# Optimization experiments

Measured on AMD Instinct MI355X. Metric: run time of the kernel, lower is better.

Reference implementation:

```python
import jax, jax.numpy as jnp
import numpy as np

B, N, DEG = 16, 1723, 8   # batch, mesh vertices, avg degree
C, L = 512, 5             # num_channels, num_layers


def _gn(x, g, b, G):
    # GroupNorm over (B, C, N), normalize per group over (C//G, N)
    Bx, Cx, Nx = x.shape
    xr = x.reshape(Bx, G, Cx // G, Nx)
    m = xr.mean(axis=(2, 3), keepdims=True)
    v = xr.var(axis=(2, 3), keepdims=True)
    xr = (xr - m) * jax.lax.rsqrt(v + 1e-5)
    return xr.reshape(Bx, Cx, Nx) * g[None, :, None] + b[None, :, None]


def _glin(W, b, x):
    # per-vertex linear: (O,I) @ (B,I,N) + b
    return jnp.einsum('oi,bin->bon', W, x) + b[None, :, None]


def _gconv(x, W, b, src, dst, w):
    # GraphConvolution: support = x^T @ W, then sparse adjacency spmm via edge list
    sup = jnp.einsum('bcn,cd->bnd', x, W)          # (B, N, C)
    msg = sup[:, src, :] * w[None, :, None]        # gather neighbors (B, E, C)
    agg = jnp.zeros_like(sup).at[:, dst, :].add(msg) + b[None, None, :]
    return agg.transpose(0, 2, 1)                  # back to (B, C, N)


def _resblock(x, p, src, dst, w):
    (pre_g, pre_b, l1W, l1b, n1g, n1b, cW, cb, n2g, n2b, l2W, l2b, skW, skb) = p
    Cin, Ch = x.shape[1], l1W.shape[0]
    y = jax.nn.relu(_gn(x, pre_g, pre_b, Cin // 8))
    y = _glin(l1W, l1b, y)
    y = jax.nn.relu(_gn(y, n1g, n1b, Ch // 8))
    y = _gconv(y, cW, cb, src, dst, w)
    y = jax.nn.relu(_gn(y, n2g, n2b, Ch // 8))
    y = _glin(l2W, l2b, y)
    if skW is not None:
        x = _glin(skW, skb, x)
    return x + y


def setup_inputs() -> dict:
    key = jax.random.key(0)
    ks = iter(jax.random.split(key, 64))
    s = 0.02
    w = lambda shp: jax.random.normal(next(ks), shp, jnp.float32) * s
    z = lambda shp: jnp.zeros(shp, jnp.float32)
    o = lambda shp: jnp.ones(shp, jnp.float32)
    H = C // 2
    E = N * DEG
    inp = {}
    inp['image_resnet'] = jax.random.normal(next(ks), (B, 2048), jnp.float32)
    inp['ref_vertices'] = jax.random.normal(next(ks), (3, N), jnp.float32)
    inp['adj_src'] = jax.random.randint(next(ks), (E,), 0, N, jnp.int32)
    inp['adj_dst'] = jnp.repeat(jnp.arange(N, dtype=jnp.int32), DEG)
    inp['adj_w'] = jnp.full((E,), 1.0 / DEG, jnp.float32)
    inp['lin0_W'] = w((2 * C, 3 + 2048)); inp['lin0_b'] = z((2 * C,))
    inp['b0_pre_g'] = o((2 * C,)); inp['b0_pre_b'] = z((2 * C,))
    inp['b0_lin1_W'] = w((H, 2 * C)); inp['b0_lin1_b'] = z((H,))
    inp['b0_n1_g'] = o((H,)); inp['b0_n1_b'] = z((H,))
    inp['b0_conv_W'] = w((H, H)); inp['b0_conv_b'] = z((H,))
    inp['b0_n2_g'] = o((H,)); inp['b0_n2_b'] = z((H,))
    inp['b0_lin2_W'] = w((C, H)); inp['b0_lin2_b'] = z((C,))
    inp['b0_skip_W'] = w((C, 2 * C)); inp['b0_skip_b'] = z((C,))
    inp['blk_pre_g'] = o((L, C)); inp['blk_pre_b'] = z((L, C))
    inp['blk_lin1_W'] = w((L, H, C)); inp['blk_lin1_b'] = z((L, H))
    inp['blk_n1_g'] = o((L, H)); inp['blk_n1_b'] = z((L, H))
    inp['blk_conv_W'] = w((L, H, H)); inp['blk_conv_b'] = z((L, H))
    inp['blk_n2_g'] = o((L, H)); inp['blk_n2_b'] = z((L, H))
    inp['blk_lin2_W'] = w((L, C, H)); inp['blk_lin2_b'] = z((L, C))
    inp['h1_W'] = w((64, C)); inp['h1_b'] = z((64,))
    inp['h2_W'] = w((32, 64)); inp['h2_b'] = z((32,))
    inp['hn_g'] = o((32,)); inp['hn_b'] = z((32,))
    inp['h3_W'] = w((3, 32)); inp['h3_b'] = z((3,))
    return inp


def reference(image_resnet, ref_vertices, adj_src, adj_dst, adj_w,
              lin0_W, lin0_b,
              b0_pre_g, b0_pre_b, b0_lin1_W, b0_lin1_b, b0_n1_g, b0_n1_b,
              b0_conv_W, b0_conv_b, b0_n2_g, b0_n2_b, b0_lin2_W, b0_lin2_b,
              b0_skip_W, b0_skip_b,
              blk_pre_g, blk_pre_b, blk_lin1_W, blk_lin1_b, blk_n1_g, blk_n1_b,
              blk_conv_W, blk_conv_b, blk_n2_g, blk_n2_b, blk_lin2_W, blk_lin2_b,
              h1_W, h1_b, h2_W, h2_b, hn_g, hn_b, h3_W, h3_b):
    Bx, Nv = image_resnet.shape[0], ref_vertices.shape[1]
    img = jnp.broadcast_to(image_resnet[:, :, None], (Bx, 2048, Nv))
    verts = jnp.broadcast_to(ref_vertices[None], (Bx, 3, Nv))
    x = jnp.concatenate([verts, img], axis=1)                 # (B, 2051, N)
    x = _glin(lin0_W, lin0_b, x)                              # (B, 1024, N)
    x = _resblock(x, (b0_pre_g, b0_pre_b, b0_lin1_W, b0_lin1_b, b0_n1_g, b0_n1_b,
                      b0_conv_W, b0_conv_b, b0_n2_g, b0_n2_b, b0_lin2_W, b0_lin2_b,
                      b0_skip_W, b0_skip_b), adj_src, adj_dst, adj_w)  # (B, 512, N)
    for i in range(blk_pre_g.shape[0]):
        x = _resblock(x, (blk_pre_g[i], blk_pre_b[i], blk_lin1_W[i], blk_lin1_b[i],
                          blk_n1_g[i], blk_n1_b[i], blk_conv_W[i], blk_conv_b[i],
                          blk_n2_g[i], blk_n2_b[i], blk_lin2_W[i], blk_lin2_b[i],
                          None, None), adj_src, adj_dst, adj_w)
    # shape decoder head
    y = jax.nn.relu(_glin(h1_W, h1_b, x))
    y = _glin(h2_W, h2_b, y)
    y = jax.nn.relu(_gn(y, hn_g, hn_b, 4))   # GroupNorm(32//8, 32)
    y = _glin(h3_W, h3_b, y)                 # (B, 3, N)
    return y
```

## Files before the change

kernel.cpp:

```cpp
#include <hip/hip_runtime.h>
#include <cstddef>
#include <cstdint>

#define THREADS 256

typedef short bh8 __attribute__((ext_vector_type(8)));
typedef float fx4 __attribute__((ext_vector_type(4)));

__device__ __forceinline__ float bf2f(unsigned short u) {
  union { unsigned int i; float f; } x;
  x.i = ((unsigned int)u) << 16;
  return x.f;
}
__device__ __forceinline__ unsigned short f2bf(float f) {
  union { float f; unsigned int i; } x;
  x.f = f;
  unsigned int r = x.i + 0x7fffu + ((x.i >> 16) & 1u);
  return (unsigned short)(r >> 16);
}

__global__ __launch_bounds__(THREADS) void transpose_img_k(
    const float* __restrict__ img, float* __restrict__ imgT) {
  int gid = blockIdx.x * THREADS + threadIdx.x;
  if (gid >= 2048 * 16) return;
  int k = gid >> 4, b = gid & 15;
  imgT[k * 16 + b] = img[b * 2048 + k];
}

__global__ __launch_bounds__(THREADS) void pack_wv_k(
    const float* __restrict__ W, float* __restrict__ wv) {
  int gid = blockIdx.x * THREADS + threadIdx.x;
  if (gid >= 3 * 1024) return;
  int k = gid >> 10, c = gid & 1023;
  wv[gid] = W[(size_t)c * 2051 + k];
}

__global__ __launch_bounds__(THREADS) void vertproj_k(
    const float* __restrict__ wv, const float* __restrict__ verts,
    float* __restrict__ v, int N) {
  int gid = blockIdx.x * THREADS + threadIdx.x;
  int c = gid & 1023, n = gid >> 10;
  if (n >= N) return;
  v[(size_t)n * 1024 + c] =
      wv[c] * verts[n] + wv[1024 + c] * verts[N + n] + wv[2048 + c] * verts[2 * N + n];
}

__global__ __launch_bounds__(THREADS) void ugemm2_k(
    const float* __restrict__ W, int ldw, int woff,
    const float* __restrict__ bias, const float* __restrict__ X,
    float* __restrict__ out, int K, int Ofull, int xl, int ks) {
  int tid = threadIdx.x;
  int b = tid & 15, cl = tid >> 4;
  int c = blockIdx.x * 16 + cl;
  int k0 = blockIdx.y * ks, k1 = k0 + ks;
  const float* wr = W + woff + (size_t)c * ldw;
  float a0 = 0.f, a1 = 0.f;
  if (xl) {
    const float* xr = X + (size_t)b * K;
    for (int k = k0; k < k1; k += 2) {
      a0 = fmaf(wr[k], xr[k], a0);
      a1 = fmaf(wr[k + 1], xr[k + 1], a1);
    }
  } else {
    for (int k = k0; k < k1; k += 2) {
      a0 = fmaf(wr[k], X[k * 16 + b], a0);
      a1 = fmaf(wr[k + 1], X[(k + 1) * 16 + b], a1);
    }
  }
  float r = a0 + a1;
  if (blockIdx.y == 0) r += bias[c];
  atomicAdd(&out[(size_t)b * Ofull + c], r);
}

struct PackDesc {
  const float* W;
  unsigned short* out;
  int O, K, TW, nOt;
  unsigned cum;
};
struct PackArgs {
  PackDesc d[8];
  unsigned grand;
};

__global__ __launch_bounds__(THREADS) void packall_k(PackArgs a) {
  unsigned gid = blockIdx.x * THREADS + threadIdx.x;
  if (gid >= a.grand) return;
  int s = 0;
#pragma unroll
  for (int i = 1; i < 8; ++i)
    if (gid >= a.d[i].cum) s = i;
#pragma unroll
  for (int i = 0; i < 8; ++i) {
    if (s != i) continue;
    const float* W = a.d[i].W;
    int O = a.d[i].O, K = a.d[i].K, TW = a.d[i].TW, nOt = a.d[i].nOt;
    unsigned e = gid - a.d[i].cum;
    int j = (int)(e & 7);
    int m = (int)((e >> 3) & 127);
    unsigned rest = e >> 10;
    int K8 = K >> 3;
    int kg = (int)(rest % (unsigned)K8);
    unsigned rest2 = rest / (unsigned)K8;
    int ot = (int)(rest2 % (unsigned)nOt);
    int l = (int)(rest2 / (unsigned)nOt);
    int o = ot * 128 + m, k = kg * 8 + j;
    float val = 0.f;
    if (o < O)
      val = TW ? W[(size_t)l * O * K + (size_t)k * O + o]
               : W[(size_t)l * O * K + (size_t)o * K + k];
    a.d[i].out[e] = f2bf(val);
  }
}

__global__ __launch_bounds__(THREADS) void vstats_k(
    const float* __restrict__ v, float* __restrict__ sv,
    float* __restrict__ sq, int N) {
  int c = blockIdx.x * THREADS + threadIdx.x;
  float s = 0.f, q = 0.f;
  for (int n = blockIdx.y; n < N; n += 16) {
    float x = v[(size_t)n * 1024 + c];
    s += x; q += x * x;
  }
  atomicAdd(&sv[c], s);
  atomicAdd(&sq[c], q);
}

__global__ __launch_bounds__(THREADS) void combine_b0_k(
    const float* __restrict__ ub, const float* __restrict__ sv,
    const float* __restrict__ sq, float* __restrict__ mean,
    float* __restrict__ rinv, int N) {
  int bg = blockIdx.x * THREADS + threadIdx.x;
  if (bg >= 2048) return;
  int b = bg >> 7, g = bg & 127;
  int c0 = g * 8;
  float fN = (float)N;
  float s = 0.f, q = 0.f;
#pragma unroll
  for (int j = 0; j < 8; ++j) {
    float u = ub[b * 1024 + c0 + j];
    float svc = sv[c0 + j];
    s += fN * u + svc;
    q += fN * u * u + 2.f * u * svc + sq[c0 + j];
  }
  float inv = 1.f / (8.f * fN);
  float m = s * inv;
  float var = q * inv - m * m;
  mean[bg] = m;
  rinv[bg] = rsqrtf(var + 1e-5f);
}

__global__ __launch_bounds__(THREADS) void agg16_k(
    const unsigned short* __restrict__ Xn, const float* __restrict__ sarr,
    const float* __restrict__ qarr, const float* __restrict__ gamma,
    const float* __restrict__ beta, const int* __restrict__ src,
    const float* __restrict__ wgt, unsigned short* __restrict__ outb, int N,
    int NPn) {
  int w = threadIdx.x >> 6, lane = threadIdx.x & 63;
  int n = blockIdx.x * 4 + w;
  if (n >= N) return;
  int b = blockIdx.y;
  int c = lane * 4;
  int g = c >> 3;
  float sfac = 1.f / (8.f * (float)N);
  float svv = sarr[b * 32 + g], qv = qarr[b * 32 + g];
  float m = svv * sfac;
  float ri = rsqrtf(qv * sfac - m * m + 1e-5f);
  float4 g4 = *(const float4*)(gamma + c);
  float4 b4 = *(const float4*)(beta + c);
  const int* sp = src + n * 8;
  const float* wp = wgt + n * 8;
  const unsigned short* base = Xn + (size_t)b * NPn * 256;
  float a0 = 0.f, a1 = 0.f, a2 = 0.f, a3 = 0.f;
#pragma unroll
  for (int j = 0; j < 8; ++j) {
    int sidx = sp[j];
    float wj = wp[j];
    ushort4 x4 = *(const ushort4*)(base + (size_t)sidx * 256 + c);
    a0 = fmaf(wj, fmaxf((bf2f(x4.x) - m) * ri * g4.x + b4.x, 0.f), a0);
    a1 = fmaf(wj, fmaxf((bf2f(x4.y) - m) * ri * g4.y + b4.y, 0.f), a1);
    a2 = fmaf(wj, fmaxf((bf2f(x4.z) - m) * ri * g4.z + b4.z, 0.f), a2);
    a3 = fmaf(wj, fmaxf((bf2f(x4.w) - m) * ri * g4.w + b4.w, 0.f), a3);
  }
  ushort4 h;
  h.x = f2bf(a0); h.y = f2bf(a1); h.z = f2bf(a2); h.w = f2bf(a3);
  *(ushort4*)(outb + ((size_t)b * NPn + n) * 256 + c) = h;
}

template <int XM, int RES, int OUT16, int ORELU, int STATS>
__global__ __launch_bounds__(THREADS) void mgemm_k(
    const unsigned short* __restrict__ Wp, const float* __restrict__ bias,
    const void* __restrict__ Xv, const float* __restrict__ ub,
    const float* __restrict__ vv, const float* __restrict__ meanS,
    const float* __restrict__ rinvS, const float* __restrict__ gamma,
    const float* __restrict__ beta, const float* __restrict__ resA,
    const float* __restrict__ resB, float* __restrict__ sacc,
    float* __restrict__ qacc, void* __restrict__ outv, int O, int I, int N,
    int NPn) {
  __shared__ unsigned short Alds[4][128][8];
  __shared__ unsigned short Blds[4][128][8];
  const int tid = threadIdx.x;
  const int lane = tid & 63;
  const int wid = tid >> 6;
  const int wm = wid & 1, wn = wid >> 1;
  const int n0 = blockIdx.x * 128;
  const int o0 = blockIdx.y * 128;
  const int b = blockIdx.z;
  const int K8 = I >> 3;
  const unsigned short* wp = Wp + (size_t)blockIdx.y * K8 * 1024;

  fx4 acc[4][4];
#pragma unroll
  for (int i = 0; i < 4; ++i)
#pragma unroll
    for (int j = 0; j < 4; ++j) {
      acc[i][j][0] = 0.f; acc[i][j][1] = 0.f;
      acc[i][j][2] = 0.f; acc[i][j][3] = 0.f;
    }

  const int ko = tid >> 6;
  const int nn = (tid & 63) * 2;
  const int mlane = lane & 15;
  const int klane = lane >> 4;

  uint4 a0r, a1r, br0, br1;
  float4 f00, f01, f10, f11, u01, u23;

  auto gload = [&](int k0) {
    const uint4* asrc = (const uint4*)(wp + (size_t)(k0 >> 3) * 1024);
    a0r = asrc[tid];
    a1r = asrc[tid + 256];
    const int ke = k0 + ko * 8;
    if (XM == 3 || XM == 4) {
      const unsigned short* p =
          (const unsigned short*)Xv + ((size_t)b * NPn + n0 + nn) * I + ke;
      br0 = *(const uint4*)p;
      br1 = *(const uint4*)(p + I);
    } else if (XM == 1) {
      const float* p = vv + (size_t)(n0 + nn) * I + ke;
      f00 = *(const float4*)p;       f01 = *(const float4*)(p + 4);
      f10 = *(const float4*)(p + I); f11 = *(const float4*)(p + I + 4);
      const float* up = ub + (size_t)b * I + ke;
      u01 = *(const float4*)up;
      u23 = *(const float4*)(up + 4);
    } else {
      const float* p = (const float*)Xv + ((size_t)b * NPn + n0 + nn) * I + ke;
      f00 = *(const float4*)p;       f01 = *(const float4*)(p + 4);
      f10 = *(const float4*)(p + I); f11 = *(const float4*)(p + I + 4);
    }
  };

  union H8 { unsigned short u[8]; uint4 q; };

  auto bstore = [&](int k0) {
    ((uint4*)&Alds[0][0][0])[tid] = a0r;
    ((uint4*)&Alds[0][0][0])[tid + 256] = a1r;
    if (XM == 4) {
      *(uint4*)&Blds[ko][nn][0] = br0;
      *(uint4*)&Blds[ko][nn + 1][0] = br1;
      return;
    }
    const int ke = k0 + ko * 8;
    float x0[8], x1[8];
    if (XM == 3) {
      H8 hr0, hr1;
      hr0.q = br0; hr1.q = br1;
#pragma unroll
      for (int j = 0; j < 8; ++j) {
        x0[j] = bf2f(hr0.u[j]);
        x1[j] = bf2f(hr1.u[j]);
      }
    } else {
      x0[0] = f00.x; x0[1] = f00.y; x0[2] = f00.z; x0[3] = f00.w;
      x0[4] = f01.x; x0[5] = f01.y; x0[6] = f01.z; x0[7] = f01.w;
      x1[0] = f10.x; x1[1] = f10.y; x1[2] = f10.z; x1[3] = f10.w;
      x1[4] = f11.x; x1[5] = f11.y; x1[6] = f11.z; x1[7] = f11.w;
    }
    if (XM == 1) {
      float uu[8] = {u01.x, u01.y, u01.z, u01.w, u23.x, u23.y, u23.z, u23.w};
#pragma unroll
      for (int j = 0; j < 8; ++j) { x0[j] += uu[j]; x1[j] += uu[j]; }
    }
    if (XM != 0) {
      float m_, r_;
      if (XM == 1) {
        m_ = meanS[b * K8 + (ke >> 3)];
        r_ = rinvS[b * K8 + (ke >> 3)];
      } else {
        float sfac = 1.f / (8.f * (float)N);
        float sv = meanS[b * K8 + (ke >> 3)];
        float qv = rinvS[b * K8 + (ke >> 3)];
        m_ = sv * sfac;
        r_ = rsqrtf(qv * sfac - m_ * m_ + 1e-5f);
      }
      float4 g0 = *(const float4*)(gamma + ke);
      float4 g1 = *(const float4*)(gamma + ke + 4);
      float4 e0 = *(const float4*)(beta + ke);
      float4 e1 = *(const float4*)(beta + ke + 4);
      float ga[8] = {g0.x, g0.y, g0.z, g0.w, g1.x, g1.y, g1.z, g1.w};
      float bb[8] = {e0.x, e0.y, e0.z, e0.w, e1.x, e1.y, e1.z, e1.w};
#pragma unroll
      for (int j = 0; j < 8; ++j) {
        x0[j] = fmaxf((x0[j] - m_) * r_ * ga[j] + bb[j], 0.f);
        x1[j] = fmaxf((x1[j] - m_) * r_ * ga[j] + bb[j], 0.f);
      }
    }
    H8 h0, h1;
#pragma unroll
    for (int j = 0; j < 8; ++j) {
      h0.u[j] = f2bf(x0[j]);
      h1.u[j] = f2bf(x1[j]);
    }
    *(uint4*)&Blds[ko][nn][0] = h0.q;
    *(uint4*)&Blds[ko][nn + 1][0] = h1.q;
  };

  gload(0);
  for (int k0 = 0; k0 < I; k0 += 32) {
    bstore(k0);
    __syncthreads();
    if (k0 + 32 < I) gload(k0 + 32);
    bh8 af[4], bfr[4];
#pragma unroll
    for (int mi = 0; mi < 4; ++mi)
      af[mi] = *(const bh8*)(&Alds[klane][wm * 64 + mi * 16 + mlane][0]);
#pragma unroll
    for (int ni = 0; ni < 4; ++ni)
      bfr[ni] = *(const bh8*)(&Blds[klane][wn * 64 + ni * 16 + mlane][0]);
#pragma unroll
    for (int mi = 0; mi < 4; ++mi)
#pragma unroll
      for (int ni = 0; ni < 4; ++ni)
        acc[mi][ni] = __builtin_amdgcn_mfma_f32_16x16x32_bf16(
            af[mi], bfr[ni], acc[mi][ni], 0, 0, 0);
    __syncthreads();
  }

  float sred[4] = {0.f, 0.f, 0.f, 0.f};
  float qred[4] = {0.f, 0.f, 0.f, 0.f};
#pragma unroll
  for (int mi = 0; mi < 4; ++mi) {
    const int o = o0 + wm * 64 + mi * 16 + klane * 4;
#pragma unroll
    for (int ni = 0; ni < 4; ++ni) {
      const int n = n0 + wn * 64 + ni * 16 + mlane;
      if (n >= N || o >= O) continue;
      float v0 = acc[mi][ni][0], v1 = acc[mi][ni][1];
      float v2 = acc[mi][ni][2], v3 = acc[mi][ni][3];
      if (bias) {
        float4 bi = *(const float4*)(bias + o);
        v0 += bi.x; v1 += bi.y; v2 += bi.z; v3 += bi.w;
      }
      size_t obase = ((size_t)b * NPn + n) * O + o;
      if (RES == 1) {
        float4 rv = *(const float4*)(resA + obase);
        v0 += rv.x; v1 += rv.y; v2 += rv.z; v3 += rv.w;
      }
      if (RES == 2) {
        float4 ra = *(const float4*)(resA + (size_t)b * O + o);
        float4 rb = *(const float4*)(resB + (size_t)n * O + o);
        v0 += ra.x + rb.x; v1 += ra.y + rb.y;
        v2 += ra.z + rb.z; v3 += ra.w + rb.w;
      }
      if (ORELU) {
        v0 = fmaxf(v0, 0.f); v1 = fmaxf(v1, 0.f);
        v2 = fmaxf(v2, 0.f); v3 = fmaxf(v3, 0.f);
      }
      if (STATS) {
        sred[mi] += v0 + v1 + v2 + v3;
        qred[mi] += v0 * v0 + v1 * v1 + v2 * v2 + v3 * v3;
      }
      if (OUT16) {
        ushort4 h;
        h.x = f2bf(v0); h.y = f2bf(v1); h.z = f2bf(v2); h.w = f2bf(v3);
        *(ushort4*)((unsigned short*)outv + obase) = h;
      } else {
        float4 fv; fv.x = v0; fv.y = v1; fv.z = v2; fv.w = v3;
        *(float4*)((float*)outv + obase) = fv;
      }
    }
  }
  if (STATS) {
    const int G = O >> 3;
#pragma unroll
    for (int mi = 0; mi < 4; ++mi) {
      const int o = o0 + wm * 64 + mi * 16 + klane * 4;
      if (o >= O) continue;
      float s = sred[mi], q = qred[mi];
#pragma unroll
      for (int m = 1; m < 16; m <<= 1) {
        s += __shfl_xor(s, m, 64);
        q += __shfl_xor(q, m, 64);
      }
      if (mlane == 0) {
        atomicAdd(&sacc[b * G + (o >> 3)], s);
        atomicAdd(&qacc[b * G + (o >> 3)], q);
      }
    }
  }
}

__global__ __launch_bounds__(THREADS) void h2_k(
    const float* __restrict__ t64, const float* __restrict__ W,
    const float* __restrict__ bias, float* __restrict__ out, int N, int NPn) {
  int gid = blockIdx.x * THREADS + threadIdx.x;
  int o = gid & 31, n = gid >> 5;
  if (n >= N) return;
  int b = blockIdx.y;
  const float* xr = t64 + ((size_t)b * NPn + n) * 64;
  const float* wr = W + o * 64;
  float acc = bias[o];
#pragma unroll
  for (int i = 0; i < 64; i += 4) {
    float4 w4 = *(const float4*)(wr + i);
    float4 x4 = *(const float4*)(xr + i);
    acc += w4.x * x4.x + w4.y * x4.y + w4.z * x4.z + w4.w * x4.w;
  }
  out[((size_t)b * NPn + n) * 32 + o] = acc;
}

__global__ __launch_bounds__(THREADS) void stats_head_k(
    const float* __restrict__ X, float* __restrict__ mean,
    float* __restrict__ rinv, int NPn, int N) {
  int b = blockIdx.x >> 2, g = blockIdx.x & 3;
  int c = g * 8 + (threadIdx.x & 7);
  float s = 0.f, q = 0.f;
  for (int n = threadIdx.x >> 3; n < N; n += 32) {
    float x = X[((size_t)b * NPn + n) * 32 + c];
    s += x; q += x * x;
  }
#pragma unroll
  for (int off = 32; off; off >>= 1) {
    s += __shfl_down(s, off, 64);
    q += __shfl_down(q, off, 64);
  }
  __shared__ float shs[4], shq[4];
  int wv = threadIdx.x >> 6;
  if ((threadIdx.x & 63) == 0) { shs[wv] = s; shq[wv] = q; }
  __syncthreads();
  if (threadIdx.x == 0) {
    s = shs[0] + shs[1] + shs[2] + shs[3];
    q = shq[0] + shq[1] + shq[2] + shq[3];
    float inv = 1.f / (8.f * (float)N);
    float m = s * inv;
    float var = q * inv - m * m;
    mean[blockIdx.x] = m;
    rinv[blockIdx.x] = rsqrtf(var + 1e-5f);
  }
}

__global__ __launch_bounds__(THREADS) void h3_k(
    const float* __restrict__ t32, const float* __restrict__ mean,
    const float* __restrict__ rinv, const float* __restrict__ g,
    const float* __restrict__ be, const float* __restrict__ W,
    const float* __restrict__ bias, float* __restrict__ out, int N, int NPn) {
  int n = blockIdx.x * THREADS + threadIdx.x;
  if (n >= N) return;
  int b = blockIdx.y;
  const float* xr = t32 + ((size_t)b * NPn + n) * 32;
  float y0 = bias[0], y1 = bias[1], y2 = bias[2];
#pragma unroll
  for (int c = 0; c < 32; ++c) {
    float m = mean[b * 4 + (c >> 3)], ri = rinv[b * 4 + (c >> 3)];
    float x = fmaxf((xr[c] - m) * ri * g[c] + be[c], 0.f);
    y0 = fmaf(W[c], x, y0);
    y1 = fmaf(W[32 + c], x, y1);
    y2 = fmaf(W[64 + c], x, y2);
  }
  out[(size_t)b * 3 * N + n] = y0;
  out[(size_t)b * 3 * N + N + n] = y1;
  out[(size_t)b * 3 * N + 2 * N + n] = y2;
}

extern "C" void kernel_launch(void* const* d_in, const int* in_sizes, int n_in,
                              void* d_out, int out_size, void* d_ws,
                              size_t ws_size, hipStream_t stream) {
  (void)n_in; (void)out_size; (void)ws_size;
  const float* img = (const float*)d_in[0];
  const float* verts = (const float*)d_in[1];
  const int* src = (const int*)d_in[2];
  const float* adjw = (const float*)d_in[4];
  const float* lin0_W = (const float*)d_in[5];
  const float* lin0_b = (const float*)d_in[6];
  const float* b0_pre_g = (const float*)d_in[7];
  const float* b0_pre_b = (const float*)d_in[8];
  const float* b0_lin1_W = (const float*)d_in[9];
  const float* b0_lin1_b = (const float*)d_in[10];
  const float* b0_n1_g = (const float*)d_in[11];
  const float* b0_n1_b = (const float*)d_in[12];
  const float* b0_conv_W = (const float*)d_in[13];
  const float* b0_conv_b = (const float*)d_in[14];
  const float* b0_n2_g = (const float*)d_in[15];
  const float* b0_n2_b = (const float*)d_in[16];
  const float* b0_lin2_W = (const float*)d_in[17];
  const float* b0_lin2_b = (const float*)d_in[18];
  const float* b0_skip_W = (const float*)d_in[19];
  const float* b0_skip_b = (const float*)d_in[20];
  const float* blk_pre_g = (const float*)d_in[21];
  const float* blk_pre_b = (const float*)d_in[22];
  const float* blk_lin1_W = (const float*)d_in[23];
  const float* blk_lin1_b = (const float*)d_in[24];
  const float* blk_n1_g = (const float*)d_in[25];
  const float* blk_n1_b = (const float*)d_in[26];
  const float* blk_conv_W = (const float*)d_in[27];
  const float* blk_conv_b = (const float*)d_in[28];
  const float* blk_n2_g = (const float*)d_in[29];
  const float* blk_n2_b = (const float*)d_in[30];
  const float* blk_lin2_W = (const float*)d_in[31];
  const float* blk_lin2_b = (const float*)d_in[32];
  const float* h1_W = (const float*)d_in[33];
  const float* h1_b = (const float*)d_in[34];
  const float* h2_W = (const float*)d_in[35];
  const float* h2_b = (const float*)d_in[36];
  const float* hn_g = (const float*)d_in[37];
  const float* hn_b = (const float*)d_in[38];
  const float* h3_W = (const float*)d_in[39];
  const float* h3_b = (const float*)d_in[40];

  const int N = in_sizes[1] / 3;
  const int NP = ((N + 127) / 128) * 128;
  const int NT128 = NP / 128;
  const int B = 16;

  char* wsb = (char*)d_ws;
  size_t off = 0;
  auto alloc = [&](size_t nbytes) {
    void* p = wsb + off;
    off += (nbytes + 255) & ~(size_t)255;
    return p;
  };
  float* xbuf = (float*)alloc((size_t)B * NP * 512 * 4);
  unsigned short* t256a = (unsigned short*)alloc((size_t)B * NP * 256 * 2);
  unsigned short* t256b = (unsigned short*)alloc((size_t)B * NP * 256 * 2);
  float* vbuf = (float*)alloc((size_t)NP * 1024 * 4);
  float* svbuf = (float*)alloc((size_t)NP * 512 * 4);
  float* t64 = (float*)alloc((size_t)B * NP * 64 * 4);
  float* t32 = (float*)alloc((size_t)B * NP * 32 * 4);
  float* imgT = (float*)alloc(2048 * 16 * 4);
  float* wv = (float*)alloc(3 * 1024 * 4);
  float* m0 = (float*)alloc(2048 * 4);
  float* r0 = (float*)alloc(2048 * 4);
  float* mh = (float*)alloc(64 * 4);
  float* rh = (float*)alloc(64 * 4);
  float* zerobuf = (float*)alloc((size_t)49152 * 4);
  float* sA = zerobuf;
  float* qA = zerobuf + 11264;
  float* sv = zerobuf + 22528;
  float* sq = zerobuf + 23552;
  float* ub = zerobuf + 24576;
  float* suT = zerobuf + 40960;
  const int off_b0n1 = 0, off_b0n2 = 512;
  auto off_pre = [](int l) { return 1024 + l * 2048; };
  auto off_n1 = [](int l) { return 1024 + l * 2048 + 1024; };
  auto off_n2 = [](int l) { return 1024 + l * 2048 + 1536; };
  unsigned short* pw_b0l1 = (unsigned short*)alloc(262144 * 2);
  unsigned short* pw_b0cv = (unsigned short*)alloc(65536 * 2);
  unsigned short* pw_b0l2 = (unsigned short*)alloc(131072 * 2);
  unsigned short* pw_b0sk = (unsigned short*)alloc(524288 * 2);
  unsigned short* pw_l1 = (unsigned short*)alloc(655360 * 2);
  unsigned short* pw_cv = (unsigned short*)alloc(327680 * 2);
  unsigned short* pw_l2 = (unsigned short*)alloc(655360 * 2);
  unsigned short* pw_h1 = (unsigned short*)alloc(65536 * 2);

  dim3 blk(THREADS);
  auto cdiv = [](size_t a, size_t b) { return (unsigned)((a + b - 1) / b); };

  hipMemsetAsync(zerobuf, 0, (size_t)49152 * 4, stream);

  {
    PackArgs pa;
    unsigned c = 0;
    auto set = [&](int i, const float* W, unsigned short* o, int O, int K,
                   int TW, int nOt, unsigned tot) {
      pa.d[i] = {W, o, O, K, TW, nOt, c};
      c += tot;
    };
    set(0, b0_lin1_W, pw_b0l1, 256, 1024, 0, 2, 262144);
    set(1, b0_conv_W, pw_b0cv, 256, 256, 1, 2, 65536);
    set(2, b0_lin2_W, pw_b0l2, 512, 256, 0, 4, 131072);
    set(3, b0_skip_W, pw_b0sk, 512, 1024, 0, 4, 524288);
    set(4, blk_lin1_W, pw_l1, 256, 512, 0, 2, 655360);
    set(5, blk_conv_W, pw_cv, 256, 256, 1, 2, 327680);
    set(6, blk_lin2_W, pw_l2, 512, 256, 0, 4, 655360);
    set(7, h1_W, pw_h1, 64, 512, 0, 1, 65536);
    pa.grand = c;
    packall_k<<<cdiv(pa.grand, THREADS), blk, 0, stream>>>(pa);
  }

  transpose_img_k<<<cdiv(2048 * 16, THREADS), blk, 0, stream>>>(img, imgT);
  pack_wv_k<<<cdiv(3072, THREADS), blk, 0, stream>>>(lin0_W, wv);
  ugemm2_k<<<dim3(64, 16), blk, 0, stream>>>(lin0_W, 2051, 3, lin0_b, imgT,
                                             ub, 2048, 1024, 0, 128);
  vertproj_k<<<cdiv((size_t)N * 1024, THREADS), blk, 0, stream>>>(wv, verts, vbuf, N);

  const dim3 aggGrid(cdiv(N, 4), 16);

  vstats_k<<<dim3(4, 16), blk, 0, stream>>>(vbuf, sv, sq, N);
  combine_b0_k<<<dim3(8), blk, 0, stream>>>(ub, sv, sq, m0, r0, N);
  mgemm_k<1, 0, 1, 0, 1><<<dim3(NT128, 2, 16), blk, 0, stream>>>(
      pw_b0l1, b0_lin1_b, nullptr, ub, vbuf, m0, r0, b0_pre_g, b0_pre_b,
      nullptr, nullptr, sA + off_b0n1, qA + off_b0n1, t256a, 256, 1024, N, NP);
  ugemm2_k<<<dim3(32, 8), blk, 0, stream>>>(b0_skip_W, 1024, 0, b0_skip_b, ub,
                                            suT, 1024, 512, 1, 128);
  mgemm_k<0, 0, 0, 0, 0><<<dim3(NT128, 4, 1), blk, 0, stream>>>(
      pw_b0sk, nullptr, vbuf, nullptr, nullptr, nullptr, nullptr, nullptr,
      nullptr, nullptr, nullptr, nullptr, nullptr, svbuf, 512, 1024, N, NP);
  agg16_k<<<aggGrid, blk, 0, stream>>>(t256a, sA + off_b0n1, qA + off_b0n1,
                                       b0_n1_g, b0_n1_b, src, adjw, t256b, N, NP);
  mgemm_k<4, 0, 1, 0, 1><<<dim3(NT128, 2, 16), blk, 0, stream>>>(
      pw_b0cv, b0_conv_b, t256b, nullptr, nullptr, nullptr, nullptr, nullptr,
      nullptr, nullptr, nullptr, sA + off_b0n2, qA + off_b0n2, t256a, 256, 256, N, NP);
  mgemm_k<3, 2, 0, 0, 1><<<dim3(NT128, 4, 16), blk, 0, stream>>>(
      pw_b0l2, b0_lin2_b, t256a, nullptr, nullptr, sA + off_b0n2, qA + off_b0n2,
      b0_n2_g, b0_n2_b, suT, svbuf, sA + off_pre(0), qA + off_pre(0), xbuf,
      512, 256, N, NP);

  for (int l = 0; l < 5; ++l) {
    const float* pg = blk_pre_g + l * 512;
    const float* pb = blk_pre_b + l * 512;
    const unsigned short* l1W = pw_l1 + (size_t)l * 131072;
    const float* l1b = blk_lin1_b + l * 256;
    const float* n1g = blk_n1_g + l * 256;
    const float* n1b = blk_n1_b + l * 256;
    const unsigned short* cW = pw_cv + (size_t)l * 65536;
    const float* cb = blk_conv_b + l * 256;
    const float* n2g = blk_n2_g + l * 256;
    const float* n2b = blk_n2_b + l * 256;
    const unsigned short* l2W = pw_l2 + (size_t)l * 131072;
    const float* l2b = blk_lin2_b + l * 512;

    mgemm_k<2, 0, 1, 0, 1><<<dim3(NT128, 2, 16), blk, 0, stream>>>(
        l1W, l1b, xbuf, nullptr, nullptr, sA + off_pre(l), qA + off_pre(l), pg,
        pb, nullptr, nullptr, sA + off_n1(l), qA + off_n1(l), t256a, 256, 512, N, NP);
    agg16_k<<<aggGrid, blk, 0, stream>>>(t256a, sA + off_n1(l), qA + off_n1(l),
                                         n1g, n1b, src, adjw, t256b, N, NP);
    mgemm_k<4, 0, 1, 0, 1><<<dim3(NT128, 2, 16), blk, 0, stream>>>(
        cW, cb, t256b, nullptr, nullptr, nullptr, nullptr, nullptr, nullptr,
        nullptr, nullptr, sA + off_n2(l), qA + off_n2(l), t256a, 256, 256, N, NP);
    if (l < 4) {
      mgemm_k<3, 1, 0, 0, 1><<<dim3(NT128, 4, 16), blk, 0, stream>>>(
          l2W, l2b, t256a, nullptr, nullptr, sA + off_n2(l), qA + off_n2(l),
          n2g, n2b, xbuf, nullptr, sA + off_pre(l + 1), qA + off_pre(l + 1),
          xbuf, 512, 256, N, NP);
    } else {
      mgemm_k<3, 1, 0, 0, 0><<<dim3(NT128, 4, 16), blk, 0, stream>>>(
          l2W, l2b, t256a, nullptr, nullptr, sA + off_n2(l), qA + off_n2(l),
          n2g, n2b, xbuf, nullptr, nullptr, nullptr, xbuf, 512, 256, N, NP);
    }
  }

  mgemm_k<0, 0, 0, 1, 0><<<dim3(NT128, 1, 16), blk, 0, stream>>>(
      pw_h1, h1_b, xbuf, nullptr, nullptr, nullptr, nullptr, nullptr, nullptr,
      nullptr, nullptr, nullptr, nullptr, t64, 64, 512, N, NP);
  h2_k<<<dim3(cdiv((size_t)N * 32, THREADS), 16), blk, 0, stream>>>(
      t64, h2_W, h2_b, t32, N, NP);
  stats_head_k<<<dim3(64), blk, 0, stream>>>(t32, mh, rh, NP, N);
  h3_k<<<dim3(cdiv(N, THREADS), 16), blk, 0, stream>>>(
      t32, mh, rh, hn_g, hn_b, h3_W, h3_b, (float*)d_out, N, NP);
}
```

Baseline: 1.411 ms.

## Double GEMM K-tile to 64 and restructure B-tile loads per column

Raises the K step of the bf16 MFMA GEMM from 32 to 64, doubling both LDS tiles and halving the number of barrier pairs per output tile. Each thread now owns one column and loads 32 contiguous K elements instead of two rows of 8, which gives longer contiguous global reads. Bias and per-batch residual loads are hoisted out of the inner epilogue loop. In exchange, each thread holds more staging registers (up to 16 float4), which may lower occupancy, and the block uses more LDS.

New measurement: 1.765 ms. 25.1% more time.

```diff
diff --git a/kernel.cpp b/kernel.cpp
--- a/kernel.cpp
+++ b/kernel.cpp
@@ -197,8 +197,8 @@
     const float* __restrict__ resB, float* __restrict__ sacc,
     float* __restrict__ qacc, void* __restrict__ outv, int O, int I, int N,
     int NPn) {
-  __shared__ unsigned short Alds[4][128][8];
-  __shared__ unsigned short Blds[4][128][8];
+  __shared__ unsigned short Alds[8][128][8];
+  __shared__ unsigned short Blds[8][128][8];
   const int tid = threadIdx.x;
   const int lane = tid & 63;
   const int wid = tid >> 6;
@@ -218,121 +218,125 @@
       acc[i][j][2] = 0.f; acc[i][j][3] = 0.f;
     }
 
-  const int ko = tid >> 6;
-  const int nn = (tid & 63) * 2;
+  const int col = tid & 127;
+  const int kgb = tid >> 7;
   const int mlane = lane & 15;
   const int klane = lane >> 4;
 
-  uint4 a0r, a1r, br0, br1;
-  float4 f00, f01, f10, f11, u01, u23;
+  uint4 ar[4], br[4];
+  float4 fr[8], ufr[8];
 
   auto gload = [&](int k0) {
     const uint4* asrc = (const uint4*)(wp + (size_t)(k0 >> 3) * 1024);
-    a0r = asrc[tid];
-    a1r = asrc[tid + 256];
-    const int ke = k0 + ko * 8;
+    ar[0] = asrc[tid];
+    ar[1] = asrc[tid + 256];
+    ar[2] = asrc[tid + 512];
+    ar[3] = asrc[tid + 768];
+    const int ke = k0 + kgb * 32;
     if (XM == 3 || XM == 4) {
       const unsigned short* p =
-          (const unsigned short*)Xv + ((size_t)b * NPn + n0 + nn) * I + ke;
-      br0 = *(const uint4*)p;
-      br1 = *(const uint4*)(p + I);
+          (const unsigned short*)Xv + ((size_t)b * NPn + n0 + col) * I + ke;
+      br[0] = *(const uint4*)p;
+      br[1] = *(const uint4*)(p + 8);
+      br[2] = *(const uint4*)(p + 16);
+      br[3] = *(const uint4*)(p + 24);
     } else if (XM == 1) {
-      const float* p = vv + (size_t)(n0 + nn) * I + ke;
-      f00 = *(const float4*)p;       f01 = *(const float4*)(p + 4);
-      f10 = *(const float4*)(p + I); f11 = *(const float4*)(p + I + 4);
+      const float* p = vv + (size_t)(n0 + col) * I + ke;
       const float* up = ub + (size_t)b * I + ke;
-      u01 = *(const float4*)up;
-      u23 = *(const float4*)(up + 4);
+#pragma unroll
+      for (int j = 0; j < 8; ++j) {
+        fr[j] = *(const float4*)(p + 4 * j);
+        ufr[j] = *(const float4*)(up + 4 * j);
+      }
     } else {
-      const float* p = (const float*)Xv + ((size_t)b * NPn + n0 + nn) * I + ke;
-      f00 = *(const float4*)p;       f01 = *(const float4*)(p + 4);
-      f10 = *(const float4*)(p + I); f11 = *(const float4*)(p + I + 4);
+      const float* p = (const float*)Xv + ((size_t)b * NPn + n0 + col) * I + ke;
+#pragma unroll
+      for (int j = 0; j < 8; ++j) fr[j] = *(const float4*)(p + 4 * j);
     }
   };
 
   union H8 { unsigned short u[8]; uint4 q; };
 
   auto bstore = [&](int k0) {
-    ((uint4*)&Alds[0][0][0])[tid] = a0r;
-    ((uint4*)&Alds[0][0][0])[tid + 256] = a1r;
+    uint4* adst = (uint4*)&Alds[0][0][0];
+    adst[tid] = ar[0];
+    adst[tid + 256] = ar[1];
+    adst[tid + 512] = ar[2];
+    adst[tid + 768] = ar[3];
     if (XM == 4) {
-      *(uint4*)&Blds[ko][nn][0] = br0;
-      *(uint4*)&Blds[ko][nn + 1][0] = br1;
+#pragma unroll
+      for (int j = 0; j < 4; ++j) *(uint4*)&Blds[kgb * 4 + j][col][0] = br[j];
       return;
     }
-    const int ke = k0 + ko * 8;
-    float x0[8], x1[8];
-    if (XM == 3) {
-      H8 hr0, hr1;
-      hr0.q = br0; hr1.q = br1;
-#pragma unroll
-      for (int j = 0; j < 8; ++j) {
-        x0[j] = bf2f(hr0.u[j]);
-        x1[j] = bf2f(hr1.u[j]);
-      }
-    } else {
-      x0[0] = f00.x; x0[1] = f00.y; x0[2] = f00.z; x0[3] = f00.w;
-      x0[4] = f01.x; x0[5] = f01.y; x0[6] = f01.z; x0[7] = f01.w;
-      x1[0] = f10.x; x1[1] = f10.y; x1[2] = f10.z; x1[3] = f10.w;
-      x1[4] = f11.x; x1[5] = f11.y; x1[6] = f11.z; x1[7] = f11.w;
-    }
-    if (XM == 1) {
-      float uu[8] = {u01.x, u01.y, u01.z, u01.w, u23.x, u23.y, u23.z, u23.w};
-#pragma unroll
-      for (int j = 0; j < 8; ++j) { x0[j] += uu[j]; x1[j] += uu[j]; }
-    }
-    if (XM != 0) {
-      float m_, r_;
+    const float sfac = 1.f / (8.f * (float)N);
+#pragma unroll
+    for (int j = 0; j < 4; ++j) {
+      const int ke = k0 + (kgb * 4 + j) * 8;
+      float x[8];
+      if (XM == 3) {
+        H8 hr; hr.q = br[j];
+#pragma unroll
+        for (int t = 0; t < 8; ++t) x[t] = bf2f(hr.u[t]);
+      } else {
+        float4 a = fr[2 * j], c = fr[2 * j + 1];
+        x[0] = a.x; x[1] = a.y; x[2] = a.z; x[3] = a.w;
+        x[4] = c.x; x[5] = c.y; x[6] = c.z; x[7] = c.w;
+      }
       if (XM == 1) {
-        m_ = meanS[b * K8 + (ke >> 3)];
-        r_ = rinvS[b * K8 + (ke >> 3)];
-      } else {
-        float sfac = 1.f / (8.f * (float)N);
-        float sv = meanS[b * K8 + (ke >> 3)];
-        float qv = rinvS[b * K8 + (ke >> 3)];
-        m_ = sv * sfac;
-        r_ = rsqrtf(qv * sfac - m_ * m_ + 1e-5f);
-      }
-      float4 g0 = *(const float4*)(gamma + ke);
-      float4 g1 = *(const float4*)(gamma + ke + 4);
-      float4 e0 = *(const float4*)(beta + ke);
-      float4 e1 = *(const float4*)(beta + ke + 4);
-      float ga[8] = {g0.x, g0.y, g0.z, g0.w, g1.x, g1.y, g1.z, g1.w};
-      float bb[8] = {e0.x, e0.y, e0.z, e0.w, e1.x, e1.y, e1.z, e1.w};
-#pragma unroll
-      for (int j = 0; j < 8; ++j) {
-        x0[j] = fmaxf((x0[j] - m_) * r_ * ga[j] + bb[j], 0.f);
-        x1[j] = fmaxf((x1[j] - m_) * r_ * ga[j] + bb[j], 0.f);
-      }
-    }
-    H8 h0, h1;
-#pragma unroll
-    for (int j = 0; j < 8; ++j) {
-      h0.u[j] = f2bf(x0[j]);
-      h1.u[j] = f2bf(x1[j]);
-    }
-    *(uint4*)&Blds[ko][nn][0] = h0.q;
-    *(uint4*)&Blds[ko][nn + 1][0] = h1.q;
+        float4 a = ufr[2 * j], c = ufr[2 * j + 1];
+        float uu[8] = {a.x, a.y, a.z, a.w, c.x, c.y, c.z, c.w};
+#pragma unroll
+        for (int t = 0; t < 8; ++t) x[t] += uu[t];
+      }
+      if (XM != 0) {
+        float m_, r_;
+        if (XM == 1) {
+          m_ = meanS[b * K8 + (ke >> 3)];
+          r_ = rinvS[b * K8 + (ke >> 3)];
+        } else {
+          float sv = meanS[b * K8 + (ke >> 3)];
+          float qv = rinvS[b * K8 + (ke >> 3)];
+          m_ = sv * sfac;
+          r_ = rsqrtf(qv * sfac - m_ * m_ + 1e-5f);
+        }
+        float4 g0 = *(const float4*)(gamma + ke);
+        float4 g1 = *(const float4*)(gamma + ke + 4);
+        float4 e0 = *(const float4*)(beta + ke);
+        float4 e1 = *(const float4*)(beta + ke + 4);
+        float ga[8] = {g0.x, g0.y, g0.z, g0.w, g1.x, g1.y, g1.z, g1.w};
+        float bb[8] = {e0.x, e0.y, e0.z, e0.w, e1.x, e1.y, e1.z, e1.w};
+#pragma unroll
+        for (int t = 0; t < 8; ++t)
+          x[t] = fmaxf((x[t] - m_) * r_ * ga[t] + bb[t], 0.f);
+      }
+      H8 h;
+#pragma unroll
+      for (int t = 0; t < 8; ++t) h.u[t] = f2bf(x[t]);
+      *(uint4*)&Blds[kgb * 4 + j][col][0] = h.q;
+    }
   };
 
   gload(0);
-  for (int k0 = 0; k0 < I; k0 += 32) {
+  for (int k0 = 0; k0 < I; k0 += 64) {
     bstore(k0);
     __syncthreads();
-    if (k0 + 32 < I) gload(k0 + 32);
-    bh8 af[4], bfr[4];
-#pragma unroll
-    for (int mi = 0; mi < 4; ++mi)
-      af[mi] = *(const bh8*)(&Alds[klane][wm * 64 + mi * 16 + mlane][0]);
-#pragma unroll
-    for (int ni = 0; ni < 4; ++ni)
-      bfr[ni] = *(const bh8*)(&Blds[klane][wn * 64 + ni * 16 + mlane][0]);
-#pragma unroll
-    for (int mi = 0; mi < 4; ++mi)
+    if (k0 + 64 < I) gload(k0 + 64);
+#pragma unroll
+    for (int c = 0; c < 2; ++c) {
+      bh8 af[4], bfr[4];
+#pragma unroll
+      for (int mi = 0; mi < 4; ++mi)
+        af[mi] = *(const bh8*)(&Alds[c * 4 + klane][wm * 64 + mi * 16 + mlane][0]);
 #pragma unroll
       for (int ni = 0; ni < 4; ++ni)
-        acc[mi][ni] = __builtin_amdgcn_mfma_f32_16x16x32_bf16(
-            af[mi], bfr[ni], acc[mi][ni], 0, 0, 0);
+        bfr[ni] = *(const bh8*)(&Blds[c * 4 + klane][wn * 64 + ni * 16 + mlane][0]);
+#pragma unroll
+      for (int mi = 0; mi < 4; ++mi)
+#pragma unroll
+        for (int ni = 0; ni < 4; ++ni)
+          acc[mi][ni] = __builtin_amdgcn_mfma_f32_16x16x32_bf16(
+              af[mi], bfr[ni], acc[mi][ni], 0, 0, 0);
+    }
     __syncthreads();
   }
 
@@ -341,23 +345,24 @@
 #pragma unroll
   for (int mi = 0; mi < 4; ++mi) {
     const int o = o0 + wm * 64 + mi * 16 + klane * 4;
+    if (o >= O) continue;
+    float4 bi;
+    if (bias) bi = *(const float4*)(bias + o);
+    float4 ra;
+    if (RES == 2) ra = *(const float4*)(resA + (size_t)b * O + o);
 #pragma unroll
     for (int ni = 0; ni < 4; ++ni) {
       const int n = n0 + wn * 64 + ni * 16 + mlane;
-      if (n >= N || o >= O) continue;
+      if (n >= N) continue;
       float v0 = acc[mi][ni][0], v1 = acc[mi][ni][1];
       float v2 = acc[mi][ni][2], v3 = acc[mi][ni][3];
-      if (bias) {
-        float4 bi = *(const float4*)(bias + o);
-        v0 += bi.x; v1 += bi.y; v2 += bi.z; v3 += bi.w;
-      }
+      if (bias) { v0 += bi.x; v1 += bi.y; v2 += bi.z; v3 += bi.w; }
       size_t obase = ((size_t)b * NPn + n) * O + o;
       if (RES == 1) {
         float4 rv = *(const float4*)(resA + obase);
         v0 += rv.x; v1 += rv.y; v2 += rv.z; v3 += rv.w;
       }
       if (RES == 2) {
-        float4 ra = *(const float4*)(resA + (size_t)b * O + o);
         float4 rb = *(const float4*)(resB + (size_t)n * O + o);
         v0 += ra.x + rb.x; v1 += ra.y + rb.y;
         v2 += ra.z + rb.z; v3 += ra.w + rb.w;
```

## Use direct global-to-LDS loads with double buffering in the MFMA GEMM

Applied to the files above, without the earlier changes.

Replaces register-staged loads of the packed weight tiles, and of bf16 activations in the XM==4 path, with global_load_lds transfers that write straight into shared memory. Double-buffers the A tile (and the B tile for XM==4) so the next K-slice is fetched while MFMAs run on the current one. The epilogue now loads bias and the per-batch residual once per row group instead of once per tile. This costs extra LDS, which may reduce occupancy, and depends on the compiler waiting correctly for the async LDS writes before the barrier.

Result: no change. 1.401 ms (-0.7%).

```diff
diff --git a/kernel.cpp b/kernel.cpp
--- a/kernel.cpp
+++ b/kernel.cpp
@@ -17,6 +17,12 @@
   x.f = f;
   unsigned int r = x.i + 0x7fffu + ((x.i >> 16) & 1u);
   return (unsigned short)(r >> 16);
+}
+
+__device__ __forceinline__ void gld16(const void* g, void* l) {
+  __builtin_amdgcn_global_load_lds(
+      (const __attribute__((address_space(1))) unsigned int*)g,
+      (__attribute__((address_space(3))) unsigned int*)l, 16, 0, 0);
 }
 
 __global__ __launch_bounds__(THREADS) void transpose_img_k(
@@ -197,8 +203,9 @@
     const float* __restrict__ resB, float* __restrict__ sacc,
     float* __restrict__ qacc, void* __restrict__ outv, int O, int I, int N,
     int NPn) {
-  __shared__ unsigned short Alds[4][128][8];
-  __shared__ unsigned short Blds[4][128][8];
+  constexpr int BBUF = (XM == 4) ? 2 : 1;
+  __shared__ unsigned short Alds[2][4][128][8];
+  __shared__ unsigned short Blds[BBUF][4][128][8];
   const int tid = threadIdx.x;
   const int lane = tid & 63;
   const int wid = tid >> 6;
@@ -218,33 +225,44 @@
       acc[i][j][2] = 0.f; acc[i][j][3] = 0.f;
     }
 
-  const int ko = tid >> 6;
-  const int nn = (tid & 63) * 2;
+  const int sko = tid >> 6;
+  const int sn = (tid & 63) * 2;
   const int mlane = lane & 15;
   const int klane = lane >> 4;
 
-  uint4 a0r, a1r, br0, br1;
+  auto dmaA = [&](int k0, int buf) {
+    const unsigned short* asrc = wp + (size_t)(k0 >> 3) * 1024;
+    unsigned short* ab = &Alds[buf][0][0][0];
+    gld16(asrc + (size_t)tid * 8, ab + (size_t)tid * 8);
+    gld16(asrc + (size_t)(tid + 256) * 8, ab + (size_t)(tid + 256) * 8);
+  };
+  auto dmaB4 = [&](int k0, int buf) {
+    const unsigned short* xs =
+        (const unsigned short*)Xv + ((size_t)b * NPn + n0) * I + k0 + wid * 8;
+    unsigned short* bb = &Blds[buf][0][0][0] + (size_t)wid * 1024;
+    gld16(xs + (size_t)lane * I, bb + (size_t)lane * 8);
+    gld16(xs + (size_t)(lane + 64) * I, bb + 512 + (size_t)lane * 8);
+  };
+
+  uint4 br0, br1;
   float4 f00, f01, f10, f11, u01, u23;
 
-  auto gload = [&](int k0) {
-    const uint4* asrc = (const uint4*)(wp + (size_t)(k0 >> 3) * 1024);
-    a0r = asrc[tid];
-    a1r = asrc[tid + 256];
-    const int ke = k0 + ko * 8;
-    if (XM == 3 || XM == 4) {
+  auto gloadB = [&](int k0) {
+    const int ke = k0 + sko * 8;
+    if (XM == 3) {
       const unsigned short* p =
-          (const unsigned short*)Xv + ((size_t)b * NPn + n0 + nn) * I + ke;
+          (const unsigned short*)Xv + ((size_t)b * NPn + n0 + sn) * I + ke;
       br0 = *(const uint4*)p;
       br1 = *(const uint4*)(p + I);
     } else if (XM == 1) {
-      const float* p = vv + (size_t)(n0 + nn) * I + ke;
+      const float* p = vv + (size_t)(n0 + sn) * I + ke;
       f00 = *(const float4*)p;       f01 = *(const float4*)(p + 4);
       f10 = *(const float4*)(p + I); f11 = *(const float4*)(p + I + 4);
       const float* up = ub + (size_t)b * I + ke;
       u01 = *(const float4*)up;
       u23 = *(const float4*)(up + 4);
-    } else {
-      const float* p = (const float*)Xv + ((size_t)b * NPn + n0 + nn) * I + ke;
+    } else if (XM == 0 || XM == 2) {
+      const float* p = (const float*)Xv + ((size_t)b * NPn + n0 + sn) * I + ke;
       f00 = *(const float4*)p;       f01 = *(const float4*)(p + 4);
       f10 = *(const float4*)(p + I); f11 = *(const float4*)(p + I + 4);
     }
@@ -252,15 +270,8 @@
 
   union H8 { unsigned short u[8]; uint4 q; };
 
-  auto bstore = [&](int k0) {
-    ((uint4*)&Alds[0][0][0])[tid] = a0r;
-    ((uint4*)&Alds[0][0][0])[tid + 256] = a1r;
-    if (XM == 4) {
-      *(uint4*)&Blds[ko][nn][0] = br0;
-      *(uint4*)&Blds[ko][nn + 1][0] = br1;
-      return;
-    }
-    const int ke = k0 + ko * 8;
+  auto bstoreB = [&](int k0) {
+    const int ke = k0 + sko * 8;
     float x0[8], x1[8];
     if (XM == 3) {
       H8 hr0, hr1;
@@ -311,29 +322,53 @@
       h0.u[j] = f2bf(x0[j]);
       h1.u[j] = f2bf(x1[j]);
     }
-    *(uint4*)&Blds[ko][nn][0] = h0.q;
-    *(uint4*)&Blds[ko][nn + 1][0] = h1.q;
+    *(uint4*)&Blds[0][sko][sn][0] = h0.q;
+    *(uint4*)&Blds[0][sko][sn + 1][0] = h1.q;
   };
 
-  gload(0);
-  for (int k0 = 0; k0 < I; k0 += 32) {
-    bstore(k0);
-    __syncthreads();
-    if (k0 + 32 < I) gload(k0 + 32);
+  auto compute = [&](int ab, int bb) {
     bh8 af[4], bfr[4];
 #pragma unroll
     for (int mi = 0; mi < 4; ++mi)
-      af[mi] = *(const bh8*)(&Alds[klane][wm * 64 + mi * 16 + mlane][0]);
+      af[mi] = *(const bh8*)(&Alds[ab][klane][wm * 64 + mi * 16 + mlane][0]);
 #pragma unroll
     for (int ni = 0; ni < 4; ++ni)
-      bfr[ni] = *(const bh8*)(&Blds[klane][wn * 64 + ni * 16 + mlane][0]);
+      bfr[ni] = *(const bh8*)(&Blds[bb][klane][wn * 64 + ni * 16 + mlane][0]);
 #pragma unroll
     for (int mi = 0; mi < 4; ++mi)
 #pragma unroll
       for (int ni = 0; ni < 4; ++ni)
         acc[mi][ni] = __builtin_amdgcn_mfma_f32_16x16x32_bf16(
             af[mi], bfr[ni], acc[mi][ni], 0, 0, 0);
+  };
+
+  if (XM == 4) {
+    dmaA(0, 0);
+    dmaB4(0, 0);
     __syncthreads();
+    for (int k0 = 0; k0 < I; k0 += 32) {
+      const int cur = (k0 >> 5) & 1;
+      if (k0 + 32 < I) {
+        dmaA(k0 + 32, cur ^ 1);
+        dmaB4(k0 + 32, cur ^ 1);
+      }
+      compute(cur, cur);
+      __syncthreads();
+    }
+  } else {
+    dmaA(0, 0);
+    gloadB(0);
+    for (int k0 = 0; k0 < I; k0 += 32) {
+      const int cur = (k0 >> 5) & 1;
+      bstoreB(k0);
+      __syncthreads();
+      if (k0 + 32 < I) {
+        dmaA(k0 + 32, cur ^ 1);
+        gloadB(k0 + 32);
+      }
+      compute(cur, 0);
+      __syncthreads();
+    }
   }
 
   float sred[4] = {0.f, 0.f, 0.f, 0.f};
@@ -341,23 +376,24 @@
 #pragma unroll
   for (int mi = 0; mi < 4; ++mi) {
     const int o = o0 + wm * 64 + mi * 16 + klane * 4;
+    if (o >= O) continue;
+    float4 bi;
+    if (bias) bi = *(const float4*)(bias + o);
+    float4 ra;
+    if (RES == 2) ra = *(const float4*)(resA + (size_t)b * O + o);
 #pragma unroll
     for (int ni = 0; ni < 4; ++ni) {
       const int n = n0 + wn * 64 + ni * 16 + mlane;
-      if (n >= N || o >= O) continue;
+      if (n >= N) continue;
       float v0 = acc[mi][ni][0], v1 = acc[mi][ni][1];
       float v2 = acc[mi][ni][2], v3 = acc[mi][ni][3];
-      if (bias) {
-        float4 bi = *(const float4*)(bias + o);
-        v0 += bi.x; v1 += bi.y; v2 += bi.z; v3 += bi.w;
-      }
+      if (bias) { v0 += bi.x; v1 += bi.y; v2 += bi.z; v3 += bi.w; }
       size_t obase = ((size_t)b * NPn + n) * O + o;
       if (RES == 1) {
         float4 rv = *(const float4*)(resA + obase);
         v0 += rv.x; v1 += rv.y; v2 += rv.z; v3 += rv.w;
       }
       if (RES == 2) {
-        float4 ra = *(const float4*)(resA + (size_t)b * O + o);
         float4 rb = *(const float4*)(resB + (size_t)n * O + o);
         v0 += ra.x + rb.x; v1 += ra.y + rb.y;
         v2 += ra.z + rb.z; v3 += ra.w + rb.w;
```
